# Kernel optimization log

Hardware: AMD Instinct MI355X
Metric: run time of the kernel (lower is better)

## Reference

```python
import jax, jax.numpy as jnp
import numpy as np

B, T, D, H = 256, 256, 384, 64  # batch, seq (BLOCK_SIZE), D_MODEL, HEAD_SIZE


def setup_inputs() -> dict:
    key = jax.random.key(0)
    k1, k2, k3, k4 = jax.random.split(key, 4)
    x = jax.random.normal(k1, (B, T, D), dtype=jnp.float32)
    # nn.Linear(D, H, bias=False): weight [H, D]; we store transposed [D, H] for x @ W
    Wq = jax.random.normal(k2, (D, H), dtype=jnp.float32) * (1.0 / np.sqrt(D))
    Wk = jax.random.normal(k3, (D, H), dtype=jnp.float32) * (1.0 / np.sqrt(D))
    Wv = jax.random.normal(k4, (D, H), dtype=jnp.float32) * (1.0 / np.sqrt(D))
    return {"x": x, "Wq": Wq, "Wk": Wk, "Wv": Wv}


def reference(x, Wq, Wk, Wv):
    # x: [B, T, D]
    q = x @ Wq  # [B, T, H]
    k = x @ Wk  # [B, T, H]
    v = x @ Wv  # [B, T, H]
    scale = 1.0 / jnp.sqrt(jnp.asarray(k.shape[-1], dtype=x.dtype))
    wei = jnp.einsum('bth,bsh->bts', q, k) * scale  # [B, T, T]
    causal = jnp.tril(jnp.ones((x.shape[1], x.shape[1]), dtype=bool))
    wei = jnp.where(causal, wei, -jnp.inf)
    wei = jax.nn.softmax(wei, axis=-1)
    # dropout is identity in eval mode (deterministic reference)
    out = jnp.einsum('bts,bsh->bth', wei, v)  # [B, T, H]
    return out
```

## Files before the change

### kernel.cpp

```cpp
#include <hip/hip_runtime.h>

#define BATCH 256
#define TT 256
#define DD 384
#define HH 64
#define SCALE 0.125f
#define SHIFT 14.0f

typedef __attribute__((ext_vector_type(8))) short short8;
typedef __attribute__((ext_vector_type(4))) float floatx4;

#define KS_STRIDE 72
#define QS_STRIDE 72
#define VT_STRIDE 264
#define PS_STRIDE 40
#define WELEMS (3 * DD * HH)

__device__ __forceinline__ unsigned short f2bf(float f) {
    unsigned int u = __float_as_uint(f);
    u += 0x7fffu + ((u >> 16) & 1u);
    return (unsigned short)(u >> 16);
}
__device__ __forceinline__ float bf2f(unsigned short u) {
    return __uint_as_float(((unsigned int)u) << 16);
}

__device__ __forceinline__ void gld_lds16(const void* g, void* ldst) {
    __builtin_amdgcn_global_load_lds(
        (__attribute__((address_space(1))) void*)(unsigned long long)g,
        (__attribute__((address_space(3))) void*)(unsigned int)(unsigned long long)ldst,
        16, 0, 0);
}

__device__ __forceinline__ short8 cvt8(float4 f0, float4 f1) {
    short8 a;
    a[0] = (short)f2bf(f0.x); a[1] = (short)f2bf(f0.y);
    a[2] = (short)f2bf(f0.z); a[3] = (short)f2bf(f0.w);
    a[4] = (short)f2bf(f1.x); a[5] = (short)f2bf(f1.y);
    a[6] = (short)f2bf(f1.z); a[7] = (short)f2bf(f1.w);
    return a;
}

__global__ void pack_w_kernel(const float* __restrict__ wq,
                              const float* __restrict__ wk,
                              const float* __restrict__ wv,
                              unsigned short* __restrict__ wf) {
    int idx = blockIdx.x * 256 + threadIdx.x;
    if (idx >= WELEMS) return;
    int j = idx & 7;
    int lane = (idx >> 3) & 63;
    int nt = (idx >> 9) & 3;
    int rem = idx >> 11;
    int mat = rem % 3;
    int ch = rem / 3;
    int l16 = lane & 15, q = lane >> 4;
    int h = 16 * nt + l16;
    int d = 32 * ch + 4 * q + (j < 4 ? j : j + 12);
    const float* w = (mat == 0) ? wq : (mat == 1) ? wk : wv;
    wf[idx] = f2bf(w[d * HH + h]);
}

__global__ __launch_bounds__(512, 2)
void fused_kernel(const float* __restrict__ x, const unsigned short* __restrict__ wfrag,
                  float* __restrict__ out) {
    __shared__ __align__(16) union LdsU {
        unsigned short w[WELEMS];
        struct {
            unsigned short ks[TT * KS_STRIDE];
            unsigned short vt[HH * VT_STRIDE];
            unsigned short q[TT * QS_STRIDE];
            unsigned short p[8][16 * PS_STRIDE];
        } s;
    } U;

    const int b = blockIdx.x;
    const int tid = threadIdx.x;
    const int wave = tid >> 6;
    const int lane = tid & 63;
    const int quad = lane >> 4;
    const int l16 = lane & 15;

    const float* xb = x + (size_t)b * TT * DD;

    const float* xr0 = xb + (size_t)(32 * wave + l16) * DD + 4 * quad;
    const float* xr1 = xr0 + (size_t)16 * DD;

    floatx4 cq[2][4] = {};
    floatx4 ck[2][4] = {};
    floatx4 cv[2][4] = {};

    float4 xP0_0, xP0_1, xP0_2, xP0_3;
    float4 xP1_0, xP1_1, xP1_2, xP1_3;
    float4 xP2_0, xP2_1, xP2_2, xP2_3;
    float4 xP3_0, xP3_1, xP3_2, xP3_3;

    #define XLOAD(B, CH)                                   \
        B##_0 = *(const float4*)(xr0 + (CH) * 32);         \
        B##_1 = *(const float4*)(xr0 + (CH) * 32 + 16);    \
        B##_2 = *(const float4*)(xr1 + (CH) * 32);         \
        B##_3 = *(const float4*)(xr1 + (CH) * 32 + 16);

    XLOAD(xP0, 0)
    XLOAD(xP1, 1)
    XLOAD(xP2, 2)
    XLOAD(xP3, 3)

    #pragma unroll
    for (int t = 0; t < 18; ++t) {
        int grp = wave * 18 + t;
        gld_lds16(wfrag + (size_t)grp * 512 + lane * 8, U.w + grp * 512);
    }

    __syncthreads();

    #define GEMM_BODY(B, CH)                                                       \
        {                                                                          \
            short8 a0 = cvt8(B##_0, B##_1);                                        \
            short8 a1 = cvt8(B##_2, B##_3);                                        \
            if ((CH) + 4 < 12) { XLOAD(B, (CH) + 4) }                              \
            const unsigned short* wb = U.w + (size_t)(CH) * 12 * 512 + lane * 8;   \
            short8 wf_[12];                                                        \
            _Pragma("unroll")                                                      \
            for (int i = 0; i < 12; ++i)                                           \
                wf_[i] = *(const short8*)(wb + (size_t)i * 512);                   \
            _Pragma("unroll")                                                      \
            for (int nt = 0; nt < 4; ++nt) {                                       \
                cq[0][nt] = __builtin_amdgcn_mfma_f32_16x16x32_bf16(a0, wf_[nt], cq[0][nt], 0, 0, 0);      \
                cq[1][nt] = __builtin_amdgcn_mfma_f32_16x16x32_bf16(a1, wf_[nt], cq[1][nt], 0, 0, 0);      \
                ck[0][nt] = __builtin_amdgcn_mfma_f32_16x16x32_bf16(a0, wf_[4 + nt], ck[0][nt], 0, 0, 0);  \
                ck[1][nt] = __builtin_amdgcn_mfma_f32_16x16x32_bf16(a1, wf_[4 + nt], ck[1][nt], 0, 0, 0);  \
                cv[0][nt] = __builtin_amdgcn_mfma_f32_16x16x32_bf16(a0, wf_[8 + nt], cv[0][nt], 0, 0, 0);  \
                cv[1][nt] = __builtin_amdgcn_mfma_f32_16x16x32_bf16(a1, wf_[8 + nt], cv[1][nt], 0, 0, 0);  \
            }                                                                      \
        }

    GEMM_BODY(xP0, 0)
    GEMM_BODY(xP1, 1)
    GEMM_BODY(xP2, 2)
    GEMM_BODY(xP3, 3)
    GEMM_BODY(xP0, 4)
    GEMM_BODY(xP1, 5)
    GEMM_BODY(xP2, 6)
    GEMM_BODY(xP3, 7)
    GEMM_BODY(xP0, 8)
    GEMM_BODY(xP1, 9)
    GEMM_BODY(xP2, 10)
    GEMM_BODY(xP3, 11)
    #undef GEMM_BODY
    #undef XLOAD

    __syncthreads();

    #pragma unroll
    for (int mi = 0; mi < 2; ++mi)
      #pragma unroll
      for (int nt = 0; nt < 4; ++nt)
        #pragma unroll
        for (int r = 0; r < 4; ++r) {
            int row = 32 * wave + 16 * mi + 4 * quad + r;
            int col = 16 * nt + l16;
            U.s.q[row * QS_STRIDE + col] = f2bf(cq[mi][nt][r]);
            U.s.ks[row * KS_STRIDE + col] = f2bf(ck[mi][nt][r]);
            U.s.vt[col * VT_STRIDE + row] = f2bf(cv[mi][nt][r]);
        }

    __syncthreads();

    floatx4 o[2][4] = {};
    float l_run[2][4] = {{0.f, 0.f, 0.f, 0.f}, {0.f, 0.f, 0.f, 0.f}};
    unsigned short* psw = U.s.p[wave];

    #pragma unroll
    for (int gi = 0; gi < 2; ++gi) {
        int g = gi ? (15 - wave) : wave;
        int gr0 = 16 * g;
        short8 aq0 = *(const short8*)(U.s.q + (size_t)(gr0 + l16) * QS_STRIDE + quad * 8);
        short8 aq1 = *(const short8*)(U.s.q + (size_t)(gr0 + l16) * QS_STRIDE + 32 + quad * 8);
        int clast = g >> 1;
        for (int c = 0; c <= clast; ++c) {
            floatx4 s[2] = {};
            #pragma unroll
            for (int ni = 0; ni < 2; ++ni) {
                const unsigned short* kbase =
                    U.s.ks + (size_t)(32 * c + 16 * ni + l16) * KS_STRIDE + quad * 8;
                s[ni] = __builtin_amdgcn_mfma_f32_16x16x32_bf16(aq0, *(const short8*)(kbase), s[ni], 0, 0, 0);
                s[ni] = __builtin_amdgcn_mfma_f32_16x16x32_bf16(aq1, *(const short8*)(kbase + 32), s[ni], 0, 0, 0);
            }
            bool partial = (c == clast);
            #pragma unroll
            for (int r = 0; r < 4; ++r) {
                int row = gr0 + 4 * quad + r;
                float p0 = __expf(s[0][r] * SCALE - SHIFT);
                float p1 = __expf(s[1][r] * SCALE - SHIFT);
                if (partial) {
                    if (32 * c + l16 > row) p0 = 0.f;
                    if (32 * c + 16 + l16 > row) p1 = 0.f;
                }
                unsigned short b0 = f2bf(p0), b1 = f2bf(p1);
                l_run[gi][r] += bf2f(b0) + bf2f(b1);
                psw[(4 * quad + r) * PS_STRIDE + l16] = b0;
                psw[(4 * quad + r) * PS_STRIDE + 16 + l16] = b1;
            }
            short8 ap = *(const short8*)(psw + l16 * PS_STRIDE + quad * 8);
            #pragma unroll
            for (int nt = 0; nt < 4; ++nt) {
                short8 bv = *(const short8*)(U.s.vt + (size_t)(16 * nt + l16) * VT_STRIDE + 32 * c + quad * 8);
                o[gi][nt] = __builtin_amdgcn_mfma_f32_16x16x32_bf16(ap, bv, o[gi][nt], 0, 0, 0);
            }
        }
    }

    float* outb = out + (size_t)b * TT * HH;
    #pragma unroll
    for (int gi = 0; gi < 2; ++gi) {
        int g = gi ? (15 - wave) : wave;
        float linv[4];
        #pragma unroll
        for (int r = 0; r < 4; ++r) {
            float l = l_run[gi][r];
            l += __shfl_xor(l, 1);
            l += __shfl_xor(l, 2);
            l += __shfl_xor(l, 4);
            l += __shfl_xor(l, 8);
            linv[r] = 1.0f / l;
        }
        #pragma unroll
        for (int nt = 0; nt < 4; ++nt)
          #pragma unroll
          for (int r = 0; r < 4; ++r) {
            int row = 16 * g + 4 * quad + r;
            outb[(size_t)row * HH + 16 * nt + l16] = o[gi][nt][r] * linv[r];
          }
    }
}

extern "C" void kernel_launch(void* const* d_in, const int* in_sizes, int n_in,
                              void* d_out, int out_size, void* d_ws, size_t ws_size,
                              hipStream_t stream) {
    const float* x  = (const float*)d_in[0];
    const float* wq = (const float*)d_in[1];
    const float* wk = (const float*)d_in[2];
    const float* wv = (const float*)d_in[3];
    unsigned short* wf = (unsigned short*)d_ws;
    float* o = (float*)d_out;

    pack_w_kernel<<<(WELEMS + 255) / 256, 256, 0, stream>>>(wq, wk, wv, wf);
    fused_kernel<<<BATCH, 512, 0, stream>>>(x, wf, o);
}
```

Measured before the change: 171.2 us.

## Halve block to 4 waves, each wave handling 64 rows and two attention tiles

The fused kernel now launches 256 threads per batch instead of 512. Each wave projects 64 rows of Q/K/V with four M-tiles sharing each weight fragment read from LDS, and processes two query row-tiles per attention pass, interleaving their MFMAs. The V transpose store becomes a single 4-element vector write. This raises per-wave register use and reuse of LDS-loaded weights, at the cost of fewer waves per block, less latency hiding, and a launch bound of one block per CU.

```diff
diff --git a/kernel.cpp b/kernel.cpp
--- a/kernel.cpp
+++ b/kernel.cpp
@@ -8,6 +8,7 @@
 #define SHIFT 14.0f
 
 typedef __attribute__((ext_vector_type(8))) short short8;
+typedef __attribute__((ext_vector_type(4))) short short4v;
 typedef __attribute__((ext_vector_type(4))) float floatx4;
 
 #define KS_STRIDE 72
@@ -60,7 +61,7 @@
     wf[idx] = f2bf(w[d * HH + h]);
 }
 
-__global__ __launch_bounds__(512, 2)
+__global__ __launch_bounds__(256, 1)
 void fused_kernel(const float* __restrict__ x, const unsigned short* __restrict__ wfrag,
                   float* __restrict__ out) {
     __shared__ __align__(16) union LdsU {
@@ -82,42 +83,48 @@
 
     const float* xb = x + (size_t)b * TT * DD;
 
-    const float* xr0 = xb + (size_t)(32 * wave + l16) * DD + 4 * quad;
+    const float* xr0 = xb + (size_t)(64 * wave + l16) * DD + 4 * quad;
     const float* xr1 = xr0 + (size_t)16 * DD;
-
-    floatx4 cq[2][4] = {};
-    floatx4 ck[2][4] = {};
-    floatx4 cv[2][4] = {};
-
-    float4 xP0_0, xP0_1, xP0_2, xP0_3;
-    float4 xP1_0, xP1_1, xP1_2, xP1_3;
-    float4 xP2_0, xP2_1, xP2_2, xP2_3;
-    float4 xP3_0, xP3_1, xP3_2, xP3_3;
+    const float* xr2 = xr0 + (size_t)32 * DD;
+    const float* xr3 = xr0 + (size_t)48 * DD;
+
+    floatx4 cq[4][4] = {};
+    floatx4 ck[4][4] = {};
+    floatx4 cv[4][4] = {};
+
+    float4 xA_0, xA_1, xA_2, xA_3, xA_4, xA_5, xA_6, xA_7;
+    float4 xB_0, xB_1, xB_2, xB_3, xB_4, xB_5, xB_6, xB_7;
+    float4 xC_0, xC_1, xC_2, xC_3, xC_4, xC_5, xC_6, xC_7;
 
     #define XLOAD(B, CH)                                   \
         B##_0 = *(const float4*)(xr0 + (CH) * 32);         \
         B##_1 = *(const float4*)(xr0 + (CH) * 32 + 16);    \
         B##_2 = *(const float4*)(xr1 + (CH) * 32);         \
-        B##_3 = *(const float4*)(xr1 + (CH) * 32 + 16);
-
-    XLOAD(xP0, 0)
-    XLOAD(xP1, 1)
-    XLOAD(xP2, 2)
-    XLOAD(xP3, 3)
+        B##_3 = *(const float4*)(xr1 + (CH) * 32 + 16);    \
+        B##_4 = *(const float4*)(xr2 + (CH) * 32);         \
+        B##_5 = *(const float4*)(xr2 + (CH) * 32 + 16);    \
+        B##_6 = *(const float4*)(xr3 + (CH) * 32);         \
+        B##_7 = *(const float4*)(xr3 + (CH) * 32 + 16);
+
+    XLOAD(xA, 0)
+    XLOAD(xB, 1)
+    XLOAD(xC, 2)
 
     #pragma unroll
-    for (int t = 0; t < 18; ++t) {
-        int grp = wave * 18 + t;
+    for (int t = 0; t < 36; ++t) {
+        int grp = wave * 36 + t;
         gld_lds16(wfrag + (size_t)grp * 512 + lane * 8, U.w + grp * 512);
     }
 
     __syncthreads();
 
-    #define GEMM_BODY(B, CH)                                                       \
+    #define GEMM_BODY(BUF, CH)                                                     \
         {                                                                          \
-            short8 a0 = cvt8(B##_0, B##_1);                                        \
-            short8 a1 = cvt8(B##_2, B##_3);                                        \
-            if ((CH) + 4 < 12) { XLOAD(B, (CH) + 4) }                              \
+            short8 a0 = cvt8(BUF##_0, BUF##_1);                                    \
+            short8 a1 = cvt8(BUF##_2, BUF##_3);                                    \
+            short8 a2 = cvt8(BUF##_4, BUF##_5);                                    \
+            short8 a3 = cvt8(BUF##_6, BUF##_7);                                    \
+            if ((CH) + 3 < 12) { XLOAD(BUF, (CH) + 3) }                            \
             const unsigned short* wb = U.w + (size_t)(CH) * 12 * 512 + lane * 8;   \
             short8 wf_[12];                                                        \
             _Pragma("unroll")                                                      \
@@ -127,109 +134,165 @@
             for (int nt = 0; nt < 4; ++nt) {                                       \
                 cq[0][nt] = __builtin_amdgcn_mfma_f32_16x16x32_bf16(a0, wf_[nt], cq[0][nt], 0, 0, 0);      \
                 cq[1][nt] = __builtin_amdgcn_mfma_f32_16x16x32_bf16(a1, wf_[nt], cq[1][nt], 0, 0, 0);      \
+                cq[2][nt] = __builtin_amdgcn_mfma_f32_16x16x32_bf16(a2, wf_[nt], cq[2][nt], 0, 0, 0);      \
+                cq[3][nt] = __builtin_amdgcn_mfma_f32_16x16x32_bf16(a3, wf_[nt], cq[3][nt], 0, 0, 0);      \
                 ck[0][nt] = __builtin_amdgcn_mfma_f32_16x16x32_bf16(a0, wf_[4 + nt], ck[0][nt], 0, 0, 0);  \
                 ck[1][nt] = __builtin_amdgcn_mfma_f32_16x16x32_bf16(a1, wf_[4 + nt], ck[1][nt], 0, 0, 0);  \
+                ck[2][nt] = __builtin_amdgcn_mfma_f32_16x16x32_bf16(a2, wf_[4 + nt], ck[2][nt], 0, 0, 0);  \
+                ck[3][nt] = __builtin_amdgcn_mfma_f32_16x16x32_bf16(a3, wf_[4 + nt], ck[3][nt], 0, 0, 0);  \
                 cv[0][nt] = __builtin_amdgcn_mfma_f32_16x16x32_bf16(a0, wf_[8 + nt], cv[0][nt], 0, 0, 0);  \
                 cv[1][nt] = __builtin_amdgcn_mfma_f32_16x16x32_bf16(a1, wf_[8 + nt], cv[1][nt], 0, 0, 0);  \
+                cv[2][nt] = __builtin_amdgcn_mfma_f32_16x16x32_bf16(a2, wf_[8 + nt], cv[2][nt], 0, 0, 0);  \
+                cv[3][nt] = __builtin_amdgcn_mfma_f32_16x16x32_bf16(a3, wf_[8 + nt], cv[3][nt], 0, 0, 0);  \
             }                                                                      \
         }
 
-    GEMM_BODY(xP0, 0)
-    GEMM_BODY(xP1, 1)
-    GEMM_BODY(xP2, 2)
-    GEMM_BODY(xP3, 3)
-    GEMM_BODY(xP0, 4)
-    GEMM_BODY(xP1, 5)
-    GEMM_BODY(xP2, 6)
-    GEMM_BODY(xP3, 7)
-    GEMM_BODY(xP0, 8)
-    GEMM_BODY(xP1, 9)
-    GEMM_BODY(xP2, 10)
-    GEMM_BODY(xP3, 11)
+    GEMM_BODY(xA, 0)
+    GEMM_BODY(xB, 1)
+    GEMM_BODY(xC, 2)
+    GEMM_BODY(xA, 3)
+    GEMM_BODY(xB, 4)
+    GEMM_BODY(xC, 5)
+    GEMM_BODY(xA, 6)
+    GEMM_BODY(xB, 7)
+    GEMM_BODY(xC, 8)
+    GEMM_BODY(xA, 9)
+    GEMM_BODY(xB, 10)
+    GEMM_BODY(xC, 11)
     #undef GEMM_BODY
     #undef XLOAD
 
     __syncthreads();
 
     #pragma unroll
-    for (int mi = 0; mi < 2; ++mi)
+    for (int m = 0; m < 4; ++m)
       #pragma unroll
-      for (int nt = 0; nt < 4; ++nt)
+      for (int nt = 0; nt < 4; ++nt) {
+        int row0 = 64 * wave + 16 * m + 4 * quad;
+        int col = 16 * nt + l16;
         #pragma unroll
         for (int r = 0; r < 4; ++r) {
-            int row = 32 * wave + 16 * mi + 4 * quad + r;
-            int col = 16 * nt + l16;
-            U.s.q[row * QS_STRIDE + col] = f2bf(cq[mi][nt][r]);
-            U.s.ks[row * KS_STRIDE + col] = f2bf(ck[mi][nt][r]);
-            U.s.vt[col * VT_STRIDE + row] = f2bf(cv[mi][nt][r]);
+            U.s.q[(row0 + r) * QS_STRIDE + col] = f2bf(cq[m][nt][r]);
+            U.s.ks[(row0 + r) * KS_STRIDE + col] = f2bf(ck[m][nt][r]);
         }
+        short4v v4;
+        v4[0] = (short)f2bf(cv[m][nt][0]);
+        v4[1] = (short)f2bf(cv[m][nt][1]);
+        v4[2] = (short)f2bf(cv[m][nt][2]);
+        v4[3] = (short)f2bf(cv[m][nt][3]);
+        *(short4v*)(U.s.vt + (size_t)col * VT_STRIDE + row0) = v4;
+      }
 
     __syncthreads();
 
-    floatx4 o[2][4] = {};
-    float l_run[2][4] = {{0.f, 0.f, 0.f, 0.f}, {0.f, 0.f, 0.f, 0.f}};
-    unsigned short* psw = U.s.p[wave];
-
-    #pragma unroll
-    for (int gi = 0; gi < 2; ++gi) {
-        int g = gi ? (15 - wave) : wave;
-        int gr0 = 16 * g;
-        short8 aq0 = *(const short8*)(U.s.q + (size_t)(gr0 + l16) * QS_STRIDE + quad * 8);
-        short8 aq1 = *(const short8*)(U.s.q + (size_t)(gr0 + l16) * QS_STRIDE + 32 + quad * 8);
-        int clast = g >> 1;
-        for (int c = 0; c <= clast; ++c) {
-            floatx4 s[2] = {};
+    float* outb = out + (size_t)b * TT * HH;
+    unsigned short* psA = U.s.p[2 * wave];
+    unsigned short* psB = U.s.p[2 * wave + 1];
+
+    #pragma unroll 1
+    for (int pass = 0; pass < 2; ++pass) {
+        const int gA = pass ? (7 - wave) : wave;
+        const int gB = pass ? (8 + wave) : (15 - wave);
+        const int grA = 16 * gA, grB = 16 * gB;
+        const int clA = gA >> 1, clB = gB >> 1;
+
+        short8 aqA0 = *(const short8*)(U.s.q + (size_t)(grA + l16) * QS_STRIDE + quad * 8);
+        short8 aqA1 = *(const short8*)(U.s.q + (size_t)(grA + l16) * QS_STRIDE + 32 + quad * 8);
+        short8 aqB0 = *(const short8*)(U.s.q + (size_t)(grB + l16) * QS_STRIDE + quad * 8);
+        short8 aqB1 = *(const short8*)(U.s.q + (size_t)(grB + l16) * QS_STRIDE + 32 + quad * 8);
+
+        floatx4 oA[4] = {}, oB[4] = {};
+        float lA[4] = {0.f, 0.f, 0.f, 0.f};
+        float lB[4] = {0.f, 0.f, 0.f, 0.f};
+
+        for (int c = 0; c <= clB; ++c) {
+            const bool doA = (c <= clA);
+            floatx4 sA[2] = {}, sB[2] = {};
             #pragma unroll
             for (int ni = 0; ni < 2; ++ni) {
                 const unsigned short* kbase =
                     U.s.ks + (size_t)(32 * c + 16 * ni + l16) * KS_STRIDE + quad * 8;
-                s[ni] = __builtin_amdgcn_mfma_f32_16x16x32_bf16(aq0, *(const short8*)(kbase), s[ni], 0, 0, 0);
-                s[ni] = __builtin_amdgcn_mfma_f32_16x16x32_bf16(aq1, *(const short8*)(kbase + 32), s[ni], 0, 0, 0);
-            }
-            bool partial = (c == clast);
-            #pragma unroll
-            for (int r = 0; r < 4; ++r) {
-                int row = gr0 + 4 * quad + r;
-                float p0 = __expf(s[0][r] * SCALE - SHIFT);
-                float p1 = __expf(s[1][r] * SCALE - SHIFT);
-                if (partial) {
-                    if (32 * c + l16 > row) p0 = 0.f;
-                    if (32 * c + 16 + l16 > row) p1 = 0.f;
+                sB[ni] = __builtin_amdgcn_mfma_f32_16x16x32_bf16(aqB0, *(const short8*)(kbase), sB[ni], 0, 0, 0);
+                sB[ni] = __builtin_amdgcn_mfma_f32_16x16x32_bf16(aqB1, *(const short8*)(kbase + 32), sB[ni], 0, 0, 0);
+            }
+            if (doA) {
+                #pragma unroll
+                for (int ni = 0; ni < 2; ++ni) {
+                    const unsigned short* kbase =
+                        U.s.ks + (size_t)(32 * c + 16 * ni + l16) * KS_STRIDE + quad * 8;
+                    sA[ni] = __builtin_amdgcn_mfma_f32_16x16x32_bf16(aqA0, *(const short8*)(kbase), sA[ni], 0, 0, 0);
+                    sA[ni] = __builtin_amdgcn_mfma_f32_16x16x32_bf16(aqA1, *(const short8*)(kbase + 32), sA[ni], 0, 0, 0);
                 }
-                unsigned short b0 = f2bf(p0), b1 = f2bf(p1);
-                l_run[gi][r] += bf2f(b0) + bf2f(b1);
-                psw[(4 * quad + r) * PS_STRIDE + l16] = b0;
-                psw[(4 * quad + r) * PS_STRIDE + 16 + l16] = b1;
-            }
-            short8 ap = *(const short8*)(psw + l16 * PS_STRIDE + quad * 8);
+            }
+            {
+                const bool partB = (c == clB);
+                #pragma unroll
+                for (int r = 0; r < 4; ++r) {
+                    int row = grB + 4 * quad + r;
+                    float p0 = __expf(sB[0][r] * SCALE - SHIFT);
+                    float p1 = __expf(sB[1][r] * SCALE - SHIFT);
+                    if (partB) {
+                        if (32 * c + l16 > row) p0 = 0.f;
+                        if (32 * c + 16 + l16 > row) p1 = 0.f;
+                    }
+                    unsigned short b0 = f2bf(p0), b1 = f2bf(p1);
+                    lB[r] += bf2f(b0) + bf2f(b1);
+                    psB[(4 * quad + r) * PS_STRIDE + l16] = b0;
+                    psB[(4 * quad + r) * PS_STRIDE + 16 + l16] = b1;
+                }
+            }
+            if (doA) {
+                const bool partA = (c == clA);
+                #pragma unroll
+                for (int r = 0; r < 4; ++r) {
+                    int row = grA + 4 * quad + r;
+                    float p0 = __expf(sA[0][r] * SCALE - SHIFT);
+                    float p1 = __expf(sA[1][r] * SCALE - SHIFT);
+                    if (partA) {
+                        if (32 * c + l16 > row) p0 = 0.f;
+                        if (32 * c + 16 + l16 > row) p1 = 0.f;
+                    }
+                    unsigned short b0 = f2bf(p0), b1 = f2bf(p1);
+                    lA[r] += bf2f(b0) + bf2f(b1);
+                    psA[(4 * quad + r) * PS_STRIDE + l16] = b0;
+                    psA[(4 * quad + r) * PS_STRIDE + 16 + l16] = b1;
+                }
+            }
+            short8 apB = *(const short8*)(psB + l16 * PS_STRIDE + quad * 8);
             #pragma unroll
             for (int nt = 0; nt < 4; ++nt) {
                 short8 bv = *(const short8*)(U.s.vt + (size_t)(16 * nt + l16) * VT_STRIDE + 32 * c + quad * 8);
-                o[gi][nt] = __builtin_amdgcn_mfma_f32_16x16x32_bf16(ap, bv, o[gi][nt], 0, 0, 0);
+                oB[nt] = __builtin_amdgcn_mfma_f32_16x16x32_bf16(apB, bv, oB[nt], 0, 0, 0);
+            }
+            if (doA) {
+                short8 apA = *(const short8*)(psA + l16 * PS_STRIDE + quad * 8);
+                #pragma unroll
+                for (int nt = 0; nt < 4; ++nt) {
+                    short8 bv = *(const short8*)(U.s.vt + (size_t)(16 * nt + l16) * VT_STRIDE + 32 * c + quad * 8);
+                    oA[nt] = __builtin_amdgcn_mfma_f32_16x16x32_bf16(apA, bv, oA[nt], 0, 0, 0);
+                }
             }
         }
-    }
-
-    float* outb = out + (size_t)b * TT * HH;
-    #pragma unroll
-    for (int gi = 0; gi < 2; ++gi) {
-        int g = gi ? (15 - wave) : wave;
-        float linv[4];
+
+        float livA[4], livB[4];
         #pragma unroll
         for (int r = 0; r < 4; ++r) {
-            float l = l_run[gi][r];
-            l += __shfl_xor(l, 1);
-            l += __shfl_xor(l, 2);
-            l += __shfl_xor(l, 4);
-            l += __shfl_xor(l, 8);
-            linv[r] = 1.0f / l;
+            float la = lA[r], lb = lB[r];
+            la += __shfl_xor(la, 1); lb += __shfl_xor(lb, 1);
+            la += __shfl_xor(la, 2); lb += __shfl_xor(lb, 2);
+            la += __shfl_xor(la, 4); lb += __shfl_xor(lb, 4);
+            la += __shfl_xor(la, 8); lb += __shfl_xor(lb, 8);
+            livA[r] = 1.0f / la;
+            livB[r] = 1.0f / lb;
         }
         #pragma unroll
         for (int nt = 0; nt < 4; ++nt)
           #pragma unroll
           for (int r = 0; r < 4; ++r) {
-            int row = 16 * g + 4 * quad + r;
-            outb[(size_t)row * HH + 16 * nt + l16] = o[gi][nt][r] * linv[r];
+            int rowA = grA + 4 * quad + r;
+            int rowB = grB + 4 * quad + r;
+            outb[(size_t)rowA * HH + 16 * nt + l16] = oA[nt][r] * livA[r];
+            outb[(size_t)rowB * HH + 16 * nt + l16] = oB[nt][r] * livB[r];
           }
     }
 }
@@ -245,5 +308,5 @@
     float* o = (float*)d_out;
 
     pack_w_kernel<<<(WELEMS + 255) / 256, 256, 0, stream>>>(wq, wk, wv, wf);
-    fused_kernel<<<BATCH, 512, 0, stream>>>(x, wf, o);
-}
+    fused_kernel<<<BATCH, 256, 0, stream>>>(x, wf, o);
+}
```

After: 177.6 us. 1.04x slower.
